# Kernel tuning notes

Hardware: AMD Instinct MI355X
Metric: run time of the kernel (lower is better)

Reference implementation:

```python
import jax, jax.numpy as jnp
import numpy as np

N_DIMS = 64
N_HALF = N_DIMS // 2
HIDDEN = 512
N_LAYERS = 8
BATCH = 16384

IDX_EVEN = np.arange(0, N_DIMS, 2)  # mask != 0 for even layers
IDX_ODD = np.arange(1, N_DIMS, 2)


def _init_mlp_params(key, n_in, n_hidden, n_out, n_layers):
    ks = jax.random.split(key, 3)
    def lin(k, fi, fo):
        return jax.random.normal(k, (n_layers, fi, fo), dtype=jnp.float32) / np.sqrt(fi)
    W1 = lin(ks[0], n_in, n_hidden)
    W2 = lin(ks[1], n_hidden, n_hidden)
    W3 = lin(ks[2], n_hidden, n_out)
    b1 = jnp.zeros((n_layers, n_hidden), jnp.float32)
    b2 = jnp.zeros((n_layers, n_hidden), jnp.float32)
    b3 = jnp.zeros((n_layers, n_out), jnp.float32)
    return W1, b1, W2, b2, W3, b3


def setup_inputs() -> dict:
    key = jax.random.key(0)
    ky, kt, ks = jax.random.split(key, 3)
    y = jax.random.normal(ky, (BATCH, N_DIMS), dtype=jnp.float32)
    tW1, tb1, tW2, tb2, tW3, tb3 = _init_mlp_params(kt, N_HALF, HIDDEN, N_HALF, N_LAYERS)
    sW1, sb1, sW2, sb2, sW3, sb3 = _init_mlp_params(ks, N_HALF, HIDDEN, N_HALF, N_LAYERS)
    s_scale = jnp.ones((N_LAYERS, N_HALF), jnp.float32)
    s_shift = jnp.zeros((N_LAYERS, N_HALF), jnp.float32)
    return {
        "y": y,
        "tW1": tW1, "tb1": tb1, "tW2": tW2, "tb2": tb2, "tW3": tW3, "tb3": tb3,
        "sW1": sW1, "sb1": sb1, "sW2": sW2, "sb2": sb2, "sW3": sW3, "sb3": sb3,
        "s_scale": s_scale, "s_shift": s_shift,
    }


def _mlp(x, W1, b1, W2, b2, W3, b3):
    h = jax.nn.relu(x @ W1 + b1)
    h = jax.nn.relu(h @ W2 + b2)
    return h @ W3 + b3


def reference(y, tW1, tb1, tW2, tb2, tW3, tb3,
              sW1, sb1, sW2, sb2, sW3, sb3, s_scale, s_shift):
    z = y
    log_det = jnp.zeros_like(y)
    for i in range(N_LAYERS):
        i0 = IDX_EVEN if i % 2 == 0 else IDX_ODD  # transformed half
        i1 = IDX_ODD if i % 2 == 0 else IDX_EVEN  # conditioning half
        z0 = z[:, i0]  # [B, 32]
        z1 = z[:, i1]  # [B, 32]
        t = _mlp(z1, tW1[i], tb1[i], tW2[i], tb2[i], tW3[i], tb3[i])
        s = jnp.tanh(_mlp(z1, sW1[i], sb1[i], sW2[i], sb2[i], sW3[i], sb3[i])) * s_scale[i] + s_shift[i]
        z0 = z0 * jnp.exp(s) + t
        z = z.at[:, i0].set(z0)
        log_det = log_det.at[:, i0].add(s)
    return z, log_det
```

## Files before the change

kernel.cpp:

```cpp
#include <hip/hip_runtime.h>

typedef unsigned short u16;
typedef unsigned int   u32;
typedef _Float16 f16;
typedef __attribute__((ext_vector_type(8))) _Float16 half8;
typedef __attribute__((ext_vector_type(4))) float f32x4;

#define NBATCH 16384

__device__ __forceinline__ u16 f2h(float x) {
  union { f16 h; u16 u; } v; v.h = (f16)x; return v.u;
}

__global__ __launch_bounds__(256) void cvt_all(
    const float* __restrict__ tW1, const float* __restrict__ sW1,
    const float* __restrict__ tW2, const float* __restrict__ sW2,
    const float* __restrict__ tW3, const float* __restrict__ sW3,
    u16* __restrict__ dW1, u16* __restrict__ dW2, u16* __restrict__ dW3)
{
  __shared__ float tile[32][33];
  const int z = blockIdx.z, bx = blockIdx.x;
  const float *tsrc, *ssrc; u16* dst; int M, N, nt, mt;
  if (bx < 16)       { tsrc = tW1; ssrc = sW1; dst = dW1; M = 32;  N = 512; nt = bx;           mt = 0; }
  else if (bx < 272) { tsrc = tW2; ssrc = sW2; dst = dW2; M = 512; N = 512; nt = (bx - 16) & 15; mt = (bx - 16) >> 4; }
  else               { tsrc = tW3; ssrc = sW3; dst = dW3; M = 512; N = 32;  nt = 0;            mt = bx - 272; }
  const float* src = ((z & 1) ? ssrc : tsrc) + (size_t)(z >> 1) * M * N;
  u16* d = dst + (size_t)z * M * N;
  const int n0 = nt * 32, m0 = mt * 32;
  for (int r = 0; r < 4; r++) {
    int m = m0 + threadIdx.y + r * 8, n = n0 + threadIdx.x;
    tile[threadIdx.y + r * 8][threadIdx.x] = src[(size_t)m * N + n];
  }
  __syncthreads();
  for (int r = 0; r < 4; r++) {
    int n = n0 + threadIdx.y + r * 8, m = m0 + threadIdx.x;
    d[(size_t)n * M + m] = f2h(tile[threadIdx.x][threadIdx.y + r * 8]);
  }
}

__global__ __launch_bounds__(512, 2) void meganvp(
    const float* __restrict__ y,
    const u16* __restrict__ W1T, const u16* __restrict__ W2T, const u16* __restrict__ W3T,
    const float* __restrict__ tb1, const float* __restrict__ sb1,
    const float* __restrict__ tb2, const float* __restrict__ sb2,
    const float* __restrict__ tb3, const float* __restrict__ sb3,
    const float* __restrict__ s_scale, const float* __restrict__ s_shift,
    float* __restrict__ out)
{
  __shared__ u16 bufA[64 * 512];
  __shared__ u16 bufB[64 * 512];
  __shared__ u16 X[64 * 40];
  __shared__ float TS[64 * 68];

  const int t = threadIdx.x;
  const int m0 = blockIdx.x * 64;
  const int lane = t & 63, w = t >> 6, lm = lane & 15, quad = lane >> 4;
  const int cw = w * 64;
  const int phase = blockIdx.x & 15;
  const int zr = t >> 3, zq = t & 7, c0 = zq * 8;

  float z[8], ld[8];
  {
    const float* yb = y + (size_t)(m0 + zr) * 64 + c0;
    f32x4 v0 = *(const f32x4*)&yb[0];
    f32x4 v1 = *(const f32x4*)&yb[4];
#pragma unroll
    for (int k = 0; k < 4; k++) { z[k] = v0[k]; z[4 + k] = v1[k]; }
#pragma unroll
    for (int e = 0; e < 8; e++) ld[e] = 0.f;
  }

  for (int layer = 0; layer < 8; layer++) {
    const int par = layer & 1;
    {
      union { u16 a[4]; uint2 v; } xv;
#pragma unroll
      for (int e = 0; e < 4; e++) xv.a[e] = f2h(z[2 * e + 1 - par]);
      *(uint2*)&X[zr * 40 + zq * 4] = xv.v;
    }
    __syncthreads();

    for (int net = 0; net < 2; net++) {
      const int idx = layer * 2 + net;

      {
        const float* b1p = (net ? sb1 : tb1) + layer * 512 + cw + quad * 4;
        f32x4 bias1[4];
#pragma unroll
        for (int ct = 0; ct < 4; ct++) bias1[ct] = *(const f32x4*)&b1p[ct * 16];
        const u16* W1p = W1T + ((size_t)idx * 512 + cw + lm) * 32 + quad * 8;
        half8 bv[4];
#pragma unroll
        for (int ct = 0; ct < 4; ct++) bv[ct] = *(const half8*)&W1p[ct * 512];
        half8 av[4];
#pragma unroll
        for (int rt = 0; rt < 4; rt++)
          av[rt] = *(const half8*)&X[(rt * 16 + lm) * 40 + quad * 8];
        f32x4 acc[4][4];
#pragma unroll
        for (int rt = 0; rt < 4; rt++)
#pragma unroll
          for (int ct = 0; ct < 4; ct++)
            acc[rt][ct] = __builtin_amdgcn_mfma_f32_16x16x32_f16(bv[ct], av[rt], bias1[ct], 0, 0, 0);
#pragma unroll
        for (int rt = 0; rt < 4; rt++) {
          const int m = rt * 16 + lm;
#pragma unroll
          for (int ct = 0; ct < 4; ct++) {
            const int n0 = cw + ct * 16 + quad * 4;
            union { u16 a[4]; uint2 v; } pk;
#pragma unroll
            for (int g = 0; g < 4; g++) {
              float v = acc[rt][ct][g];
              pk.a[g] = f2h(v > 0.f ? v : 0.f);
            }
            *(uint2*)&bufA[m * 512 + ((((n0 >> 3) ^ (m & 7)) << 3) | (n0 & 7))] = pk.v;
          }
        }
      }
      __syncthreads();

      {
        const float* b2p = (net ? sb2 : tb2) + layer * 512 + cw + quad * 4;
        f32x4 acc[4][4];
#pragma unroll
        for (int ct = 0; ct < 4; ct++) {
          const f32x4 b = *(const f32x4*)&b2p[ct * 16];
#pragma unroll
          for (int rt = 0; rt < 4; rt++) acc[rt][ct] = b;
        }
        const u16* W2p = W2T + ((size_t)idx * 512 + cw + lm) * 512 + quad * 8;
        half8 bb[3][4];
#pragma unroll
        for (int p = 0; p < 3; p++) {
          const int kp = ((p + phase) & 15) * 32;
#pragma unroll
          for (int ct = 0; ct < 4; ct++)
            bb[p][ct] = *(const half8*)&W2p[ct * 8192 + kp];
        }
        half8 av[2][4];
        {
          const int kk0 = (phase & 15) * 32;
#pragma unroll
          for (int rt = 0; rt < 4; rt++) {
            const int m = rt * 16 + lm;
            av[0][rt] = *(const half8*)&bufA[m * 512 + ((((kk0 >> 3) + quad) ^ (m & 7)) << 3)];
          }
        }
#pragma unroll
        for (int ci = 0; ci < 16; ci++) {
          if (ci < 15) {
            const int kk1 = ((ci + 1 + phase) & 15) * 32;
#pragma unroll
            for (int rt = 0; rt < 4; rt++) {
              const int m = rt * 16 + lm;
              av[(ci + 1) & 1][rt] = *(const half8*)&bufA[m * 512 + ((((kk1 >> 3) + quad) ^ (m & 7)) << 3)];
            }
          }
#pragma unroll
          for (int rt = 0; rt < 4; rt++)
#pragma unroll
            for (int ct = 0; ct < 4; ct++)
              acc[rt][ct] = __builtin_amdgcn_mfma_f32_16x16x32_f16(bb[ci % 3][ct], av[ci & 1][rt], acc[rt][ct], 0, 0, 0);
          if (ci < 13) {
            const int kn = ((ci + 3 + phase) & 15) * 32;
#pragma unroll
            for (int ct = 0; ct < 4; ct++)
              bb[ci % 3][ct] = *(const half8*)&W2p[ct * 8192 + kn];
          }
        }
#pragma unroll
        for (int rt = 0; rt < 4; rt++) {
          const int m = rt * 16 + lm;
#pragma unroll
          for (int ct = 0; ct < 4; ct++) {
            const int n0 = cw + ct * 16 + quad * 4;
            union { u16 a[4]; uint2 v; } pk;
#pragma unroll
            for (int g = 0; g < 4; g++) {
              float v = acc[rt][ct][g];
              pk.a[g] = f2h(v > 0.f ? v : 0.f);
            }
            *(uint2*)&bufB[m * 512 + ((((n0 >> 3) ^ (m & 7)) << 3) | (n0 & 7))] = pk.v;
          }
        }
      }
      __syncthreads();

      {
        const int hr = (w & 3) * 16, hc = (w >> 2) * 16;
        const u16* W3p = W3T + ((size_t)idx * 32 + hc + lm) * 512 + quad * 8;
        const int j0 = hc + quad * 4;
        f32x4 ha[2];
        ha[0] = net ? *(const f32x4*)&sb3[layer * 32 + j0]
                    : *(const f32x4*)&tb3[layer * 32 + j0];
        ha[1] = (f32x4){0.f, 0.f, 0.f, 0.f};
        const int m = hr + lm;
        half8 pv[4];
#pragma unroll
        for (int p = 0; p < 4; p++)
          pv[p] = *(const half8*)&W3p[((p + phase) & 15) * 32];
        half8 avh[2];
        {
          const int kk0 = (phase & 15) * 32;
          avh[0] = *(const half8*)&bufB[m * 512 + ((((kk0 >> 3) + quad) ^ (m & 7)) << 3)];
        }
#pragma unroll
        for (int ci = 0; ci < 16; ci++) {
          if (ci < 15) {
            const int kk1 = ((ci + 1 + phase) & 15) * 32;
            avh[(ci + 1) & 1] = *(const half8*)&bufB[m * 512 + ((((kk1 >> 3) + quad) ^ (m & 7)) << 3)];
          }
          ha[ci & 1] = __builtin_amdgcn_mfma_f32_16x16x32_f16(pv[ci & 3], avh[ci & 1], ha[ci & 1], 0, 0, 0);
          if (ci < 12)
            pv[ci & 3] = *(const half8*)&W3p[((ci + 4 + phase) & 15) * 32];
        }
        if (net == 0) {
#pragma unroll
          for (int g = 0; g < 4; g++)
            TS[m * 68 + 2 * (j0 + g)] = ha[0][g] + ha[1][g];
        } else {
          const f32x4 sc = *(const f32x4*)&s_scale[layer * 32 + j0];
          const f32x4 sh = *(const f32x4*)&s_shift[layer * 32 + j0];
#pragma unroll
          for (int g = 0; g < 4; g++)
            TS[m * 68 + 2 * (j0 + g) + 1] = tanhf(ha[0][g] + ha[1][g]) * sc[g] + sh[g];
        }
      }
      __syncthreads();
    }

    {
      const float* base = &TS[zr * 68 + zq * 8];
      f32x4 q0 = *(const f32x4*)&base[0];
      f32x4 q1 = *(const f32x4*)&base[4];
      float q[8];
#pragma unroll
      for (int k = 0; k < 4; k++) { q[k] = q0[k]; q[4 + k] = q1[k]; }
#pragma unroll
      for (int e = 0; e < 4; e++) {
        const float tv = q[2 * e], sv = q[2 * e + 1];
        const int zi = 2 * e + par;
        z[zi] = z[zi] * expf(sv) + tv;
        ld[zi] += sv;
      }
    }
  }

  {
    float* zb = out + (size_t)(m0 + zr) * 64 + c0;
    float* lb = out + (size_t)NBATCH * 64 + (size_t)(m0 + zr) * 64 + c0;
    f32x4 v0, v1, l0, l1;
#pragma unroll
    for (int k = 0; k < 4; k++) {
      v0[k] = z[k]; v1[k] = z[4 + k];
      l0[k] = ld[k]; l1[k] = ld[4 + k];
    }
    *(f32x4*)&zb[0] = v0; *(f32x4*)&zb[4] = v1;
    *(f32x4*)&lb[0] = l0; *(f32x4*)&lb[4] = l1;
  }
}

extern "C" void kernel_launch(void* const* d_in, const int* in_sizes, int n_in,
                              void* d_out, int out_size, void* d_ws, size_t ws_size,
                              hipStream_t stream) {
  (void)in_sizes; (void)n_in; (void)out_size; (void)ws_size;
  const float* y   = (const float*)d_in[0];
  const float* tW1 = (const float*)d_in[1];
  const float* tb1 = (const float*)d_in[2];
  const float* tW2 = (const float*)d_in[3];
  const float* tb2 = (const float*)d_in[4];
  const float* tW3 = (const float*)d_in[5];
  const float* tb3 = (const float*)d_in[6];
  const float* sW1 = (const float*)d_in[7];
  const float* sb1 = (const float*)d_in[8];
  const float* sW2 = (const float*)d_in[9];
  const float* sb2 = (const float*)d_in[10];
  const float* sW3 = (const float*)d_in[11];
  const float* sb3 = (const float*)d_in[12];
  const float* s_scale = (const float*)d_in[13];
  const float* s_shift = (const float*)d_in[14];
  float* out = (float*)d_out;

  char* ws = (char*)d_ws;
  const size_t W1SZ = (size_t)16 * 512 * 32 * 2;
  const size_t W2SZ = (size_t)16 * 512 * 512 * 2;
  u16* W1 = (u16*)(ws);
  u16* W2 = (u16*)(ws + W1SZ);
  u16* W3 = (u16*)(ws + W1SZ + W2SZ);

  cvt_all<<<dim3(288, 1, 16), dim3(32, 8), 0, stream>>>(tW1, sW1, tW2, sW2, tW3, sW3,
                                                        W1, W2, W3);

  meganvp<<<256, 512, 0, stream>>>(y, W1, W2, W3, tb1, sb1, tb2, sb2, tb3, sb3,
                                   s_scale, s_shift, out);
}
```

Measured before the change: 434.2 us.

## Use 1024-thread blocks with 16 waves each owning 32 hidden columns

Doubles the block size from 512 to 1024 threads so each of 16 waves computes 32 hidden columns instead of 64, halving per-wave accumulators and weight registers. The per-thread coupling state shrinks to 4 elements, and the third-layer GEMV runs only on the first 8 waves. The double-buffered LDS activation prefetch in the second GEMM is removed in favour of loading activations just in time. The aim is more waves resident per CU to hide memory latency, at the cost of idle waves in the output stage, less software pipelining, and 1024-thread barriers.

```diff
diff --git a/kernel.cpp b/kernel.cpp
--- a/kernel.cpp
+++ b/kernel.cpp
@@ -38,7 +38,7 @@
   }
 }
 
-__global__ __launch_bounds__(512, 2) void meganvp(
+__global__ __launch_bounds__(1024, 1) void meganvp(
     const float* __restrict__ y,
     const u16* __restrict__ W1T, const u16* __restrict__ W2T, const u16* __restrict__ W3T,
     const float* __restrict__ tb1, const float* __restrict__ sb1,
@@ -55,28 +55,25 @@
   const int t = threadIdx.x;
   const int m0 = blockIdx.x * 64;
   const int lane = t & 63, w = t >> 6, lm = lane & 15, quad = lane >> 4;
-  const int cw = w * 64;
+  const int cw = w * 32;
   const int phase = blockIdx.x & 15;
-  const int zr = t >> 3, zq = t & 7, c0 = zq * 8;
-
-  float z[8], ld[8];
+  const int zr = t >> 4, zc0 = (t & 15) * 4;
+
+  float z[4], ld[4];
   {
-    const float* yb = y + (size_t)(m0 + zr) * 64 + c0;
-    f32x4 v0 = *(const f32x4*)&yb[0];
-    f32x4 v1 = *(const f32x4*)&yb[4];
-#pragma unroll
-    for (int k = 0; k < 4; k++) { z[k] = v0[k]; z[4 + k] = v1[k]; }
-#pragma unroll
-    for (int e = 0; e < 8; e++) ld[e] = 0.f;
+    const float* yb = y + (size_t)(m0 + zr) * 64 + zc0;
+    f32x4 v = *(const f32x4*)yb;
+#pragma unroll
+    for (int k = 0; k < 4; k++) { z[k] = v[k]; ld[k] = 0.f; }
   }
 
   for (int layer = 0; layer < 8; layer++) {
     const int par = layer & 1;
     {
-      union { u16 a[4]; uint2 v; } xv;
-#pragma unroll
-      for (int e = 0; e < 4; e++) xv.a[e] = f2h(z[2 * e + 1 - par]);
-      *(uint2*)&X[zr * 40 + zq * 4] = xv.v;
+      union { u16 a[2]; u32 v; } xv;
+      xv.a[0] = f2h(z[1 - par]);
+      xv.a[1] = f2h(z[3 - par]);
+      *(u32*)&X[zr * 40 + (zc0 >> 1)] = xv.v;
     }
     __syncthreads();
 
@@ -85,28 +82,28 @@
 
       {
         const float* b1p = (net ? sb1 : tb1) + layer * 512 + cw + quad * 4;
-        f32x4 bias1[4];
-#pragma unroll
-        for (int ct = 0; ct < 4; ct++) bias1[ct] = *(const f32x4*)&b1p[ct * 16];
+        f32x4 bias1[2];
+#pragma unroll
+        for (int ct = 0; ct < 2; ct++) bias1[ct] = *(const f32x4*)&b1p[ct * 16];
         const u16* W1p = W1T + ((size_t)idx * 512 + cw + lm) * 32 + quad * 8;
-        half8 bv[4];
-#pragma unroll
-        for (int ct = 0; ct < 4; ct++) bv[ct] = *(const half8*)&W1p[ct * 512];
+        half8 bv[2];
+#pragma unroll
+        for (int ct = 0; ct < 2; ct++) bv[ct] = *(const half8*)&W1p[ct * 512];
         half8 av[4];
 #pragma unroll
         for (int rt = 0; rt < 4; rt++)
           av[rt] = *(const half8*)&X[(rt * 16 + lm) * 40 + quad * 8];
-        f32x4 acc[4][4];
+        f32x4 acc[4][2];
 #pragma unroll
         for (int rt = 0; rt < 4; rt++)
 #pragma unroll
-          for (int ct = 0; ct < 4; ct++)
+          for (int ct = 0; ct < 2; ct++)
             acc[rt][ct] = __builtin_amdgcn_mfma_f32_16x16x32_f16(bv[ct], av[rt], bias1[ct], 0, 0, 0);
 #pragma unroll
         for (int rt = 0; rt < 4; rt++) {
           const int m = rt * 16 + lm;
 #pragma unroll
-          for (int ct = 0; ct < 4; ct++) {
+          for (int ct = 0; ct < 2; ct++) {
             const int n0 = cw + ct * 16 + quad * 4;
             union { u16 a[4]; uint2 v; } pk;
 #pragma unroll
@@ -122,50 +119,40 @@
 
       {
         const float* b2p = (net ? sb2 : tb2) + layer * 512 + cw + quad * 4;
-        f32x4 acc[4][4];
-#pragma unroll
-        for (int ct = 0; ct < 4; ct++) {
+        f32x4 acc[4][2];
+#pragma unroll
+        for (int ct = 0; ct < 2; ct++) {
           const f32x4 b = *(const f32x4*)&b2p[ct * 16];
 #pragma unroll
           for (int rt = 0; rt < 4; rt++) acc[rt][ct] = b;
         }
         const u16* W2p = W2T + ((size_t)idx * 512 + cw + lm) * 512 + quad * 8;
-        half8 bb[3][4];
+        half8 bb[3][2];
 #pragma unroll
         for (int p = 0; p < 3; p++) {
           const int kp = ((p + phase) & 15) * 32;
 #pragma unroll
-          for (int ct = 0; ct < 4; ct++)
+          for (int ct = 0; ct < 2; ct++)
             bb[p][ct] = *(const half8*)&W2p[ct * 8192 + kp];
         }
-        half8 av[2][4];
-        {
-          const int kk0 = (phase & 15) * 32;
+#pragma unroll
+        for (int ci = 0; ci < 16; ci++) {
+          const int kk = ((ci + phase) & 15) * 32;
+          half8 av[4];
 #pragma unroll
           for (int rt = 0; rt < 4; rt++) {
             const int m = rt * 16 + lm;
-            av[0][rt] = *(const half8*)&bufA[m * 512 + ((((kk0 >> 3) + quad) ^ (m & 7)) << 3)];
-          }
-        }
-#pragma unroll
-        for (int ci = 0; ci < 16; ci++) {
-          if (ci < 15) {
-            const int kk1 = ((ci + 1 + phase) & 15) * 32;
-#pragma unroll
-            for (int rt = 0; rt < 4; rt++) {
-              const int m = rt * 16 + lm;
-              av[(ci + 1) & 1][rt] = *(const half8*)&bufA[m * 512 + ((((kk1 >> 3) + quad) ^ (m & 7)) << 3)];
-            }
+            av[rt] = *(const half8*)&bufA[m * 512 + ((((kk >> 3) + quad) ^ (m & 7)) << 3)];
           }
 #pragma unroll
           for (int rt = 0; rt < 4; rt++)
 #pragma unroll
-            for (int ct = 0; ct < 4; ct++)
-              acc[rt][ct] = __builtin_amdgcn_mfma_f32_16x16x32_f16(bb[ci % 3][ct], av[ci & 1][rt], acc[rt][ct], 0, 0, 0);
+            for (int ct = 0; ct < 2; ct++)
+              acc[rt][ct] = __builtin_amdgcn_mfma_f32_16x16x32_f16(bb[ci % 3][ct], av[rt], acc[rt][ct], 0, 0, 0);
           if (ci < 13) {
             const int kn = ((ci + 3 + phase) & 15) * 32;
 #pragma unroll
-            for (int ct = 0; ct < 4; ct++)
+            for (int ct = 0; ct < 2; ct++)
               bb[ci % 3][ct] = *(const half8*)&W2p[ct * 8192 + kn];
           }
         }
@@ -173,7 +160,7 @@
         for (int rt = 0; rt < 4; rt++) {
           const int m = rt * 16 + lm;
 #pragma unroll
-          for (int ct = 0; ct < 4; ct++) {
+          for (int ct = 0; ct < 2; ct++) {
             const int n0 = cw + ct * 16 + quad * 4;
             union { u16 a[4]; uint2 v; } pk;
 #pragma unroll
@@ -187,7 +174,7 @@
       }
       __syncthreads();
 
-      {
+      if (w < 8) {
         const int hr = (w & 3) * 16, hc = (w >> 2) * 16;
         const u16* W3p = W3T + ((size_t)idx * 32 + hc + lm) * 512 + quad * 8;
         const int j0 = hc + quad * 4;
@@ -231,33 +218,20 @@
     }
 
     {
-      const float* base = &TS[zr * 68 + zq * 8];
-      f32x4 q0 = *(const f32x4*)&base[0];
-      f32x4 q1 = *(const f32x4*)&base[4];
-      float q[8];
-#pragma unroll
-      for (int k = 0; k < 4; k++) { q[k] = q0[k]; q[4 + k] = q1[k]; }
-#pragma unroll
-      for (int e = 0; e < 4; e++) {
-        const float tv = q[2 * e], sv = q[2 * e + 1];
-        const int zi = 2 * e + par;
-        z[zi] = z[zi] * expf(sv) + tv;
-        ld[zi] += sv;
-      }
+      f32x4 q = *(const f32x4*)&TS[zr * 68 + zc0];
+      z[par]     = z[par]     * expf(q[1]) + q[0];  ld[par]     += q[1];
+      z[2 + par] = z[2 + par] * expf(q[3]) + q[2];  ld[2 + par] += q[3];
     }
   }
 
   {
-    float* zb = out + (size_t)(m0 + zr) * 64 + c0;
-    float* lb = out + (size_t)NBATCH * 64 + (size_t)(m0 + zr) * 64 + c0;
-    f32x4 v0, v1, l0, l1;
-#pragma unroll
-    for (int k = 0; k < 4; k++) {
-      v0[k] = z[k]; v1[k] = z[4 + k];
-      l0[k] = ld[k]; l1[k] = ld[4 + k];
-    }
-    *(f32x4*)&zb[0] = v0; *(f32x4*)&zb[4] = v1;
-    *(f32x4*)&lb[0] = l0; *(f32x4*)&lb[4] = l1;
+    float* zb = out + (size_t)(m0 + zr) * 64 + zc0;
+    float* lb = out + (size_t)NBATCH * 64 + (size_t)(m0 + zr) * 64 + zc0;
+    f32x4 v0, l0;
+#pragma unroll
+    for (int k = 0; k < 4; k++) { v0[k] = z[k]; l0[k] = ld[k]; }
+    *(f32x4*)zb = v0;
+    *(f32x4*)lb = l0;
   }
 }
 
@@ -292,6 +266,6 @@
   cvt_all<<<dim3(288, 1, 16), dim3(32, 8), 0, stream>>>(tW1, sW1, tW2, sW2, tW3, sW3,
                                                         W1, W2, W3);
 
-  meganvp<<<256, 512, 0, stream>>>(y, W1, W2, W3, tb1, sb1, tb2, sb2, tb3, sb3,
-                                   s_scale, s_shift, out);
-}
+  meganvp<<<256, 1024, 0, stream>>>(y, W1, W2, W3, tb1, sb1, tb2, sb2, tb3, sb3,
+                                    s_scale, s_shift, out);
+}
```

Result: no change. 438.5 us (+1.0%).
